# Performance work log

Measured on AMD Instinct MI355X. Metric: run time of the kernel, lower is better.

Reference implementation:

```python
import jax, jax.numpy as jnp
import numpy as np

H = 4096
D = 104
# segment boundaries for the 10 log_softmax groups
SEG = [0, 13, 26, 39, 48, 52, 65, 78, 91, 100, 104]

def setup_inputs() -> dict:
    key = jax.random.key(0)
    ks = jax.random.split(key, 8)
    s_h = 1.0 / np.sqrt(H)
    s_d = 1.0 / np.sqrt(D)
    return {
        "line": jax.random.normal(ks[0], (D,), jnp.float32),
        "hidden": jax.random.normal(ks[1], (H,), jnp.float32),
        "Uw": jax.random.uniform(ks[2], (H, H), jnp.float32, -s_h, s_h),
        "Ub": jax.random.uniform(ks[3], (H,), jnp.float32, -s_h, s_h),
        "Ww": jax.random.uniform(ks[4], (H, D), jnp.float32, -s_d, s_d),
        "Wb": jax.random.uniform(ks[5], (H,), jnp.float32, -s_d, s_d),
        "Vw": jax.random.uniform(ks[6], (D, H), jnp.float32, -s_h, s_h),
        "Vb": jax.random.uniform(ks[7], (D,), jnp.float32, -s_h, s_h),
    }

def reference(line, hidden, Uw, Ub, Ww, Wb, Vw, Vb):
    # h_t = sigmoid(U(hidden) + W(line))
    h_t = jax.nn.sigmoid(Uw @ hidden + Ub + Ww @ line + Wb)  # [H]
    pred = Vw @ h_t + Vb  # [D]
    # segmented log_softmax over the 10 fixed groups, then concat
    pred_logsoft = jnp.concatenate(
        [jax.nn.log_softmax(pred[a:b]) for a, b in zip(SEG[:-1], SEG[1:])]
    )
    return pred_logsoft, h_t
```

## Files before the change

kernel.cpp:

```cpp
#include <hip/hip_runtime.h>
#include <math.h>

#define H 4096
#define D 104

__global__ void __launch_bounds__(256) k_hidden(
    const float* __restrict__ Uw, const float* __restrict__ hidden,
    const float* __restrict__ Ub, const float* __restrict__ Ww,
    const float* __restrict__ line, const float* __restrict__ Wb,
    float* __restrict__ h_out)
{
    const int wave = threadIdx.x >> 6;
    const int lane = threadIdx.x & 63;
    const int row  = blockIdx.x * 4 + wave;

    const float4* __restrict__ u  = (const float4*)(Uw + (size_t)row * H);
    const float4* __restrict__ hv = (const float4*)hidden;

    float acc = 0.f;
    #pragma unroll 4
    for (int j4 = lane; j4 < H / 4; j4 += 64) {
        float4 a = u[j4];
        float4 b = hv[j4];
        acc += a.x * b.x + a.y * b.y + a.z * b.z + a.w * b.w;
    }

    const float4* __restrict__ w  = (const float4*)(Ww + (size_t)row * D);
    const float4* __restrict__ lv = (const float4*)line;
    if (lane < D / 4) {
        float4 a = w[lane];
        float4 b = lv[lane];
        acc += a.x * b.x + a.y * b.y + a.z * b.z + a.w * b.w;
    }

    #pragma unroll
    for (int off = 32; off; off >>= 1)
        acc += __shfl_down(acc, off, 64);

    if (lane == 0) {
        float v = acc + Ub[row] + Wb[row];
        h_out[row] = 1.f / (1.f + expf(-v));
    }
}

__global__ void __launch_bounds__(832) k_pred(
    const float* __restrict__ Vw, const float* __restrict__ h_t,
    const float* __restrict__ Vb, float* __restrict__ out)
{
    __shared__ float s_pred[13];
    const int seg_a[11] = {0, 13, 26, 39, 48, 52, 65, 78, 91, 100, 104};

    const int s    = blockIdx.x;
    const int a    = seg_a[s];
    const int len  = seg_a[s + 1] - a;
    const int wave = threadIdx.x >> 6;
    const int lane = threadIdx.x & 63;

    if (wave < len) {
        const int d = a + wave;
        const float4* __restrict__ v  = (const float4*)(Vw + (size_t)d * H);
        const float4* __restrict__ hv = (const float4*)h_t;
        float acc = 0.f;
        #pragma unroll 4
        for (int j4 = lane; j4 < H / 4; j4 += 64) {
            float4 x = v[j4];
            float4 y = hv[j4];
            acc += x.x * y.x + x.y * y.y + x.z * y.z + x.w * y.w;
        }
        #pragma unroll
        for (int off = 32; off; off >>= 1)
            acc += __shfl_down(acc, off, 64);
        if (lane == 0) s_pred[wave] = acc + Vb[d];
    }
    __syncthreads();

    if (wave == 0) {
        float x = (lane < len) ? s_pred[lane] : -INFINITY;
        float m = x;
        #pragma unroll
        for (int off = 32; off; off >>= 1)
            m = fmaxf(m, __shfl_xor(m, off, 64));
        float e = (lane < len) ? expf(x - m) : 0.f;
        float ssum = e;
        #pragma unroll
        for (int off = 32; off; off >>= 1)
            ssum += __shfl_xor(ssum, off, 64);
        if (lane < len) out[a + lane] = x - m - logf(ssum);
    }
}

extern "C" void kernel_launch(void* const* d_in, const int* in_sizes, int n_in,
                              void* d_out, int out_size, void* d_ws, size_t ws_size,
                              hipStream_t stream) {
    const float* line   = (const float*)d_in[0];
    const float* hidden = (const float*)d_in[1];
    const float* Uw     = (const float*)d_in[2];
    const float* Ub     = (const float*)d_in[3];
    const float* Ww     = (const float*)d_in[4];
    const float* Wb     = (const float*)d_in[5];
    const float* Vw     = (const float*)d_in[6];
    const float* Vb     = (const float*)d_in[7];

    float* out = (float*)d_out;
    float* h_t = out + D;

    k_hidden<<<H / 4, 256, 0, stream>>>(Uw, hidden, Ub, Ww, line, Wb, h_t);
    k_pred<<<10, 832, 0, stream>>>(Vw, h_t, Vb, out);
}
```

Measured before the change: 22.58 us.

## Split prediction GEMV across one block per row and separate log-softmax kernel

The fused prediction kernel, which ran only 10 blocks (one per segment), is replaced by a GEMV with one 256-thread block per output row (104 blocks), so the Vw read is spread over many more compute units. A third tiny kernel then does the segmented log_softmax from a workspace buffer. This adds an extra kernel launch and a global round trip for the 104 predictions in exchange for wider parallelism.

Result: faster. 21.90 us (-3.0%).

```diff
diff --git a/kernel.cpp b/kernel.cpp
--- a/kernel.cpp
+++ b/kernel.cpp
@@ -43,50 +43,55 @@
     }
 }
 
-__global__ void __launch_bounds__(832) k_pred(
+__global__ void __launch_bounds__(256) k_pred_rows(
     const float* __restrict__ Vw, const float* __restrict__ h_t,
-    const float* __restrict__ Vb, float* __restrict__ out)
+    const float* __restrict__ Vb, float* __restrict__ pred)
 {
-    __shared__ float s_pred[13];
+    __shared__ float r[4];
+    const int d    = blockIdx.x;
+    const int tid  = threadIdx.x;
+    const int wave = tid >> 6;
+    const int lane = tid & 63;
+
+    const float4* __restrict__ v  = (const float4*)(Vw + (size_t)d * H);
+    const float4* __restrict__ hv = (const float4*)h_t;
+
+    float acc = 0.f;
+    #pragma unroll
+    for (int j4 = tid; j4 < H / 4; j4 += 256) {
+        float4 x = v[j4];
+        float4 y = hv[j4];
+        acc += x.x * y.x + x.y * y.y + x.z * y.z + x.w * y.w;
+    }
+    #pragma unroll
+    for (int off = 32; off; off >>= 1)
+        acc += __shfl_down(acc, off, 64);
+    if (lane == 0) r[wave] = acc;
+    __syncthreads();
+    if (tid == 0)
+        pred[d] = r[0] + r[1] + r[2] + r[3] + Vb[d];
+}
+
+__global__ void __launch_bounds__(640) k_logsoftmax(
+    const float* __restrict__ pred, float* __restrict__ out)
+{
     const int seg_a[11] = {0, 13, 26, 39, 48, 52, 65, 78, 91, 100, 104};
-
-    const int s    = blockIdx.x;
+    const int s    = threadIdx.x >> 6;
+    const int lane = threadIdx.x & 63;
     const int a    = seg_a[s];
     const int len  = seg_a[s + 1] - a;
-    const int wave = threadIdx.x >> 6;
-    const int lane = threadIdx.x & 63;
 
-    if (wave < len) {
-        const int d = a + wave;
-        const float4* __restrict__ v  = (const float4*)(Vw + (size_t)d * H);
-        const float4* __restrict__ hv = (const float4*)h_t;
-        float acc = 0.f;
-        #pragma unroll 4
-        for (int j4 = lane; j4 < H / 4; j4 += 64) {
-            float4 x = v[j4];
-            float4 y = hv[j4];
-            acc += x.x * y.x + x.y * y.y + x.z * y.z + x.w * y.w;
-        }
-        #pragma unroll
-        for (int off = 32; off; off >>= 1)
-            acc += __shfl_down(acc, off, 64);
-        if (lane == 0) s_pred[wave] = acc + Vb[d];
-    }
-    __syncthreads();
-
-    if (wave == 0) {
-        float x = (lane < len) ? s_pred[lane] : -INFINITY;
-        float m = x;
-        #pragma unroll
-        for (int off = 32; off; off >>= 1)
-            m = fmaxf(m, __shfl_xor(m, off, 64));
-        float e = (lane < len) ? expf(x - m) : 0.f;
-        float ssum = e;
-        #pragma unroll
-        for (int off = 32; off; off >>= 1)
-            ssum += __shfl_xor(ssum, off, 64);
-        if (lane < len) out[a + lane] = x - m - logf(ssum);
-    }
+    float x = (lane < len) ? pred[a + lane] : -INFINITY;
+    float m = x;
+    #pragma unroll
+    for (int off = 32; off; off >>= 1)
+        m = fmaxf(m, __shfl_xor(m, off, 64));
+    float e = (lane < len) ? expf(x - m) : 0.f;
+    float ssum = e;
+    #pragma unroll
+    for (int off = 32; off; off >>= 1)
+        ssum += __shfl_xor(ssum, off, 64);
+    if (lane < len) out[a + lane] = x - m - logf(ssum);
 }
 
 extern "C" void kernel_launch(void* const* d_in, const int* in_sizes, int n_in,
@@ -101,9 +106,11 @@
     const float* Vw     = (const float*)d_in[6];
     const float* Vb     = (const float*)d_in[7];
 
-    float* out = (float*)d_out;
-    float* h_t = out + D;
+    float* out  = (float*)d_out;
+    float* h_t  = out + D;
+    float* pred = (float*)d_ws;
 
     k_hidden<<<H / 4, 256, 0, stream>>>(Uw, hidden, Ub, Ww, line, Wb, h_t);
-    k_pred<<<10, 832, 0, stream>>>(Vw, h_t, Vb, out);
+    k_pred_rows<<<D, 256, 0, stream>>>(Vw, h_t, Vb, pred);
+    k_logsoftmax<<<1, 640, 0, stream>>>(pred, out);
 }
```
